# Optimization experiments

Measured on AMD Instinct MI355X. Metric: run time of the kernel, lower is better.

Reference implementation:

```python
import jax, jax.numpy as jnp
import numpy as np

N, E, H, S, F = 50000, 800000, 96, 48, 24


def _mlp(x, W1, b1, W2, b2):
    # equinox MLP depth=1: Linear -> relu -> Linear (identity final activation)
    h = jax.nn.relu(x @ W1.T + b1)
    return h @ W2.T + b2


def _segment_softmax(scores, seg, num_segments):
    mx = jax.ops.segment_max(scores, seg, num_segments=num_segments)
    e = jnp.exp(scores - mx[seg])
    s = jax.ops.segment_sum(e, seg, num_segments=num_segments)
    return e / (s[seg] + 1e-9)


def setup_inputs() -> dict:
    key = jax.random.key(0)
    ks = jax.random.split(key, 32)
    def p(i, shape):
        return jax.random.normal(ks[i], shape, dtype=jnp.float32) * 0.05
    in_attn = 2 * H + 2 * S + F   # 312
    w_attn = 2 * H                # 192
    gin = 3 * H                   # 288
    inp = {
        "x": p(0, (N, H)),
        "x_s": p(1, (N, S)),
        "edge_features": p(2, (E, F)),
        "edge_index": jax.random.randint(ks[3], (2, E), 0, N),
        # fwd attention MLP: in_attn -> w_attn -> 1
        "fwd_W1": p(4, (w_attn, in_attn)), "fwd_b1": p(5, (w_attn,)),
        "fwd_W2": p(6, (1, w_attn)), "fwd_b2": p(7, (1,)),
        # rev gate MLP: in_attn -> w_attn -> 1
        "rev_W1": p(8, (w_attn, in_attn)), "rev_b1": p(9, (w_attn,)),
        "rev_W2": p(10, (1, w_attn)), "rev_b2": p(11, (1,)),
        # reset gate MLP: 3H -> 3H -> H
        "reset_W1": p(12, (gin, gin)), "reset_b1": p(13, (gin,)),
        "reset_W2": p(14, (H, gin)), "reset_b2": p(15, (H,)),
        # update gate MLP: 3H -> 3H -> H
        "update_W1": p(16, (gin, gin)), "update_b1": p(17, (gin,)),
        "update_W2": p(18, (H, gin)), "update_b2": p(19, (H,)),
        # candidate MLP: 3H -> 3H -> H
        "cand_W1": p(20, (gin, gin)), "cand_b1": p(21, (gin,)),
        "cand_W2": p(22, (H, gin)), "cand_b2": p(23, (H,)),
    }
    return inp


def reference(x, x_s, edge_features, edge_index,
              fwd_W1, fwd_b1, fwd_W2, fwd_b2,
              rev_W1, rev_b1, rev_W2, rev_b2,
              reset_W1, reset_b1, reset_W2, reset_b2,
              update_W1, update_b1, update_W2, update_b2,
              cand_W1, cand_b1, cand_W2, cand_b2):
    num_nodes = x.shape[0]
    src, dest = edge_index[0], edge_index[1]

    def compute_messages(s, d, W1, b1, W2, b2, use_softmax):
        feat = jnp.concatenate([x[s], x[d], x_s[s], x_s[d], edge_features], axis=-1)
        raw = _mlp(feat, W1, b1, W2, b2)[:, 0]  # [E]
        if use_softmax:
            raw = jax.nn.leaky_relu(raw) / jnp.sqrt(jnp.asarray(x.shape[-1], dtype=x.dtype))
            w = _segment_softmax(raw, d, num_nodes)
        else:
            w = jax.nn.sigmoid(raw)
        agg = jax.ops.segment_sum(x[s] * w[:, None], d, num_segments=num_nodes)
        return agg, w

    fwd_msgs, fwd_w = compute_messages(src, dest, fwd_W1, fwd_b1, fwd_W2, fwd_b2, True)
    rev_msgs, rev_w = compute_messages(dest, src, rev_W1, rev_b1, rev_W2, rev_b2, False)

    messages = jnp.concatenate([fwd_msgs, rev_msgs], axis=-1)  # [N, 2H]
    gate_input = jnp.concatenate([x, messages], axis=-1)        # [N, 3H]
    r_gate = jax.nn.sigmoid(_mlp(gate_input, reset_W1, reset_b1, reset_W2, reset_b2))
    z_gate = jax.nn.sigmoid(_mlp(gate_input, update_W1, update_b1, update_W2, update_b2))
    cand_input = jnp.concatenate([r_gate * x, messages], axis=-1)
    candidate = jnp.tanh(_mlp(cand_input, cand_W1, cand_b1, cand_W2, cand_b2))
    update = (1 - z_gate) * x + z_gate * candidate
    return (update, fwd_w, rev_w, z_gate, r_gate)
```

## Files before the change

kernel.cpp:

```cpp
#include <hip/hip_runtime.h>
#include <math.h>

typedef unsigned short u16;
typedef unsigned int   u32;

#define HDIM 96
#define SDIM 48
#define FDIM 24
#define KA   312
#define WATT 192
#define KG   288

#define AS_E  328
#define KT_A  10
#define KT_G  9
#define NS    296

#define NFRAG (2 * KT_A * 12 * 64)
#define W1F_Q (KT_G * 18 * 64)
#define W2F_Q (KT_G * 6 * 64)
#define NODEF_Q (3 * (W1F_Q + W2F_Q))

typedef __attribute__((ext_vector_type(8))) __bf16 bf16x8;
typedef __attribute__((ext_vector_type(4))) float  f32x4;

__device__ __forceinline__ u16 f2bf(float f) {
  u32 u = __float_as_uint(f);
  u = (u + 0x7FFFu + ((u >> 16) & 1u)) >> 16;
  return (u16)u;
}
__device__ __forceinline__ float bf2f(u16 v) {
  return __uint_as_float((u32)v << 16);
}
__device__ __forceinline__ u32 pack2(float a, float b) {
  return (u32)f2bf(a) | ((u32)f2bf(b) << 16);
}
__device__ __forceinline__ f32x4 mfma_bf16(bf16x8 a, bf16x8 b, f32x4 c) {
  return __builtin_amdgcn_mfma_f32_16x16x32_bf16(a, b, c, 0, 0, 0);
}

__global__ __launch_bounds__(256) void w_prep(
    const float* __restrict__ fW1, const float* __restrict__ rW1,
    uint4* __restrict__ Bfrag)
{
  const int idx = blockIdx.x * 256 + threadIdx.x;
  if (idx >= NFRAG) return;
  const int lane = idx & 63;
  const int frag = idx >> 6;
  const int nt   = frag % 12;
  const int rest = frag / 12;
  const int kt   = rest % KT_A;
  const int mlp  = rest / KT_A;
  const int q = lane >> 4, c = lane & 15;
  const int n  = nt * 16 + c;
  const int p0 = kt * 16 + q * 4;
  const float* W = mlp ? rW1 : fW1;
  u32 v[4];
#pragma unroll
  for (int w = 0; w < 4; ++w) {
    const int p = p0 + w;
    u32 val = 0u;
    if (p < 156) {
      int src = p;
      if (mlp) {
        if (src < 48)       src += 48;
        else if (src < 96)  src -= 48;
        else if (src < 120) src += 24;
        else if (src < 144) src -= 24;
      }
      const float2 wv = *(const float2*)(W + (size_t)n * KA + 2 * src);
      val = pack2(wv.x, wv.y);
    }
    v[w] = val;
  }
  Bfrag[idx] = make_uint4(v[0], v[1], v[2], v[3]);
}

__global__ __launch_bounds__(256) void w_prep_node(
    const float* __restrict__ W, uint4* __restrict__ outf, int NT)
{
  const int nfrag = KT_G * NT * 64;
  const int idx = blockIdx.x * 256 + threadIdx.x;
  if (idx >= nfrag) return;
  const int lane = idx & 63;
  const int frag = idx >> 6;
  const int nt = frag % NT, kt = frag / NT;
  const int q = lane >> 4, c = lane & 15;
  const int n = nt * 16 + c;
  const int k0 = kt * 32 + q * 8;
  u32 v[4];
#pragma unroll
  for (int w = 0; w < 4; ++w) {
    const float2 wv = *(const float2*)(W + (size_t)n * KG + k0 + 2 * w);
    v[w] = pack2(wv.x, wv.y);
  }
  outf[idx] = make_uint4(v[0], v[1], v[2], v[3]);
}

__global__ __launch_bounds__(256) void x_prep(
    const float* __restrict__ x, const float* __restrict__ xs,
    u32* __restrict__ xb, u32* __restrict__ xsb, int N)
{
  const int i = blockIdx.x * 256 + threadIdx.x;
  const int nx = N * 48;
  if (i < nx) {
    const float2 v = ((const float2*)x)[i];
    xb[i] = pack2(v.x, v.y);
  } else if (i < nx + N * 24) {
    const float2 v = ((const float2*)xs)[i - nx];
    xsb[i - nx] = pack2(v.x, v.y);
  }
}

__global__ __launch_bounds__(256, 2) void edge_kernel(
    const u32* __restrict__ xb, const u32* __restrict__ xsb,
    const float* __restrict__ ef, const int* __restrict__ ei,
    const u16* __restrict__ Bfrag,
    const float* __restrict__ fb1, const float* __restrict__ fW2,
    const float* __restrict__ fb2,
    const float* __restrict__ rb1, const float* __restrict__ rW2,
    const float* __restrict__ rb2,
    float* __restrict__ pe, float* __restrict__ out_revw, int N, int E)
{
  __shared__ __align__(16) u16 Alds[64 * AS_E];
  __shared__ float red[4][64];

  const int tid  = threadIdx.x;
  const int wave = tid >> 6, lane = tid & 63;
  const int q = lane >> 4, c = lane & 15;
  const int e0 = blockIdx.x * 64;

  {
    const int el = tid >> 2, sub = tid & 3;
    const int e = min(e0 + el, E - 1);
    int s = ei[e], d = ei[(size_t)E + e];
    s = min(max(s, 0), N - 1); d = min(max(d, 0), N - 1);
    const uint4* xsr = (const uint4*)(xb  + (size_t)s * 48);
    const uint4* xdr = (const uint4*)(xb  + (size_t)d * 48);
    const uint4* ssr = (const uint4*)(xsb + (size_t)s * 24);
    const uint4* sdr = (const uint4*)(xsb + (size_t)d * 24);
    uint4* Arow = (uint4*)&Alds[el * AS_E];
    uint4 v[10];
    if (sub == 0) {
#pragma unroll
      for (int i = 0; i < 10; ++i) v[i] = xsr[i];
    } else if (sub == 1) {
      v[0] = xsr[10]; v[1] = xsr[11];
#pragma unroll
      for (int i = 0; i < 8; ++i) v[2 + i] = xdr[i];
    } else if (sub == 2) {
#pragma unroll
      for (int i = 0; i < 4; ++i) v[i] = xdr[8 + i];
#pragma unroll
      for (int i = 0; i < 6; ++i) v[4 + i] = ssr[i];
    } else {
#pragma unroll
      for (int i = 0; i < 6; ++i) v[i] = sdr[i];
      const float4* efr = (const float4*)(ef + (size_t)e * 24);
#pragma unroll
      for (int u = 0; u < 3; ++u) {
        const float4 a = efr[2 * u], b = efr[2 * u + 1];
        v[6 + u] = make_uint4(pack2(a.x, a.y), pack2(a.z, a.w),
                              pack2(b.x, b.y), pack2(b.z, b.w));
      }
      v[9] = make_uint4(0u, 0u, 0u, 0u);
    }
#pragma unroll
    for (int i = 0; i < 10; ++i) Arow[sub * 10 + i] = v[i];
  }
  __syncthreads();

  const bf16x8* __restrict__ Bf = (const bf16x8*)Bfrag;

  for (int mlp = 0; mlp < 2; ++mlp) {
    f32x4 acc[4][3];
#pragma unroll
    for (int m = 0; m < 4; ++m)
      for (int t = 0; t < 3; ++t)
        acc[m][t] = (f32x4){0.f, 0.f, 0.f, 0.f};

#pragma unroll
    for (int kt = 0; kt < KT_A; ++kt) {
      bf16x8 a[4];
#pragma unroll
      for (int m = 0; m < 4; ++m)
        a[m] = *(const bf16x8*)&Alds[(m * 16 + c) * AS_E + kt * 32 + q * 8];
#pragma unroll
      for (int t = 0; t < 3; ++t) {
        const bf16x8 b =
            Bf[(((mlp * KT_A + kt) * 12) + wave * 3 + t) * 64 + lane];
#pragma unroll
        for (int m = 0; m < 4; ++m)
          acc[m][t] = mfma_bf16(a[m], b, acc[m][t]);
      }
    }

    const float* b1p = mlp ? rb1 : fb1;
    const float* W2p = mlp ? rW2 : fW2;
    float p[4][4];
#pragma unroll
    for (int m = 0; m < 4; ++m)
      for (int r = 0; r < 4; ++r) p[m][r] = 0.f;
#pragma unroll
    for (int t = 0; t < 3; ++t) {
      const int n = (wave * 3 + t) * 16 + c;
      const float b1f = b1p[n];
      const float w2f = W2p[n];
#pragma unroll
      for (int m = 0; m < 4; ++m)
        for (int r = 0; r < 4; ++r) {
          float h = acc[m][t][r] + b1f;
          h = h > 0.f ? h : 0.f;
          p[m][r] += h * w2f;
        }
    }
    for (int off = 1; off <= 8; off <<= 1)
#pragma unroll
      for (int m = 0; m < 4; ++m)
        for (int r = 0; r < 4; ++r)
          p[m][r] += __shfl_xor(p[m][r], off, 64);

    __syncthreads();
    if (c == 0) {
#pragma unroll
      for (int m = 0; m < 4; ++m)
        for (int r = 0; r < 4; ++r)
          red[wave][m * 16 + q * 4 + r] = p[m][r];
    }
    __syncthreads();

    if (tid < 64 && e0 + tid < E) {
      float raw = red[0][tid] + red[1][tid] + red[2][tid] + red[3][tid];
      const int e = e0 + tid;
      if (mlp == 0) {
        raw += fb2[0];
        const float lr = raw > 0.f ? raw : 0.01f * raw;
        pe[e] = __expf(lr * 0.10206207261596575f);
      } else {
        raw += rb2[0];
        out_revw[e] = 1.f / (1.f + __expf(-raw));
      }
    }
  }
}

__global__ __launch_bounds__(256) void k_hist(
    const int* __restrict__ ei, int* __restrict__ deg_d,
    int* __restrict__ deg_s, int N, int E)
{
  const int e = blockIdx.x * 256 + threadIdx.x;
  if (e >= E) return;
  const int s = min(max(ei[e], 0), N - 1);
  const int d = min(max(ei[(size_t)E + e], 0), N - 1);
  atomicAdd(&deg_d[d], 1);
  atomicAdd(&deg_s[s], 1);
}

__global__ __launch_bounds__(256) void k_scan1(
    const int* __restrict__ deg_d, const int* __restrict__ deg_s,
    int* __restrict__ start_d, int* __restrict__ start_s,
    int* __restrict__ bsum_d, int* __restrict__ bsum_s, int N)
{
  __shared__ int sh[256];
  const int t = threadIdx.x, i = blockIdx.x * 256 + t;
  {
    const int v = (i < N) ? deg_d[i] : 0;
    sh[t] = v; __syncthreads();
    for (int off = 1; off < 256; off <<= 1) {
      const int u = (t >= off) ? sh[t - off] : 0;
      __syncthreads();
      sh[t] += u;
      __syncthreads();
    }
    if (i < N) start_d[i] = sh[t] - v;
    if (t == 255) bsum_d[blockIdx.x] = sh[255];
    __syncthreads();
  }
  {
    const int v = (i < N) ? deg_s[i] : 0;
    sh[t] = v; __syncthreads();
    for (int off = 1; off < 256; off <<= 1) {
      const int u = (t >= off) ? sh[t - off] : 0;
      __syncthreads();
      sh[t] += u;
      __syncthreads();
    }
    if (i < N) start_s[i] = sh[t] - v;
    if (t == 255) bsum_s[blockIdx.x] = sh[255];
  }
}

__global__ void k_scan2(int* bsum_d, int* bsum_s, int nb) {
  if (threadIdx.x == 0) {
    int r = 0;
    for (int b = 0; b < nb; ++b) { const int t = bsum_d[b]; bsum_d[b] = r; r += t; }
  } else if (threadIdx.x == 1) {
    int r = 0;
    for (int b = 0; b < nb; ++b) { const int t = bsum_s[b]; bsum_s[b] = r; r += t; }
  }
}

__global__ __launch_bounds__(256) void k_scan3(
    int* __restrict__ start_d, int* __restrict__ start_s,
    const int* __restrict__ bsum_d, const int* __restrict__ bsum_s,
    int* __restrict__ pos_d, int* __restrict__ pos_s, int N)
{
  const int i = blockIdx.x * 256 + threadIdx.x;
  if (i >= N) return;
  const int b = i >> 8;
  const int vd = start_d[i] + bsum_d[b]; start_d[i] = vd; pos_d[i] = vd;
  const int vs = start_s[i] + bsum_s[b]; start_s[i] = vs; pos_s[i] = vs;
}

__global__ __launch_bounds__(256) void k_fill(
    const int* __restrict__ ei, int* __restrict__ pos_d,
    int* __restrict__ pos_s, int* __restrict__ eidx_d,
    int* __restrict__ eidx_s, int N, int E)
{
  const int e = blockIdx.x * 256 + threadIdx.x;
  if (e >= E) return;
  const int s = min(max(ei[e], 0), N - 1);
  const int d = min(max(ei[(size_t)E + e], 0), N - 1);
  eidx_d[atomicAdd(&pos_d[d], 1)] = e;
  eidx_s[atomicAdd(&pos_s[s], 1)] = e;
}

template <int DIR>
__global__ __launch_bounds__(256) void k_agg(
    const float* __restrict__ x, const int* __restrict__ ei,
    const float* __restrict__ pe, const float* __restrict__ revw,
    const int* __restrict__ start, const int* __restrict__ endp,
    const int* __restrict__ eidx,
    u16* __restrict__ outm, float* __restrict__ out_fwdw, int N, int E)
{
  const int g = threadIdx.x >> 5;
  const int l = threadIdx.x & 31;
  const int n = blockIdx.x * 8 + g;
  if (n >= N) return;
  const int beg = start[n], end = endp[n];

  float inv = 1.f;
  if (DIR == 0) {
    float sum = 0.f;
    for (int i = beg + l; i < end; i += 32) sum += pe[eidx[i]];
    for (int off = 16; off; off >>= 1) sum += __shfl_xor(sum, off, 32);
    inv = 1.f / (sum + 1e-9f);
    for (int i = beg + l; i < end; i += 32) {
      const int e = eidx[i];
      out_fwdw[e] = pe[e] * inv;
    }
  }

  float a0 = 0.f, a1 = 0.f, a2 = 0.f;
  for (int i = beg; i < end; ++i) {
    const int e = eidx[i];
    const float w = (DIR == 0) ? pe[e] * inv : revw[e];
    const int o = (DIR == 0) ? min(max(ei[e], 0), N - 1)
                             : min(max(ei[(size_t)E + e], 0), N - 1);
    const float* xr = x + (size_t)o * 96;
    a0 += w * xr[l];
    a1 += w * xr[l + 32];
    a2 += w * xr[l + 64];
  }
  u16* orow = outm + (size_t)n * 96;
  orow[l] = f2bf(a0); orow[l + 32] = f2bf(a1); orow[l + 64] = f2bf(a2);
}

__device__ __forceinline__ void node_mlp(
    const u16* __restrict__ Alds, u16* __restrict__ Hlds,
    const bf16x8* __restrict__ W1f, const bf16x8* __restrict__ W2f,
    const float* __restrict__ b1,
    int wave, int lane, int q, int c, int ntc, int ntc2,
    f32x4 (&acc2)[4][2])
{
  f32x4 acc[4][5];
#pragma unroll
  for (int m = 0; m < 4; ++m)
    for (int t = 0; t < 5; ++t) acc[m][t] = (f32x4){0.f, 0.f, 0.f, 0.f};

#pragma unroll
  for (int kt = 0; kt < KT_G; ++kt) {
    bf16x8 a[4];
#pragma unroll
    for (int m = 0; m < 4; ++m)
      a[m] = *(const bf16x8*)&Alds[(m * 16 + c) * NS + kt * 32 + q * 8];
#pragma unroll
    for (int t = 0; t < 5; ++t) {
      if (t < ntc) {
        const int nt = wave + 4 * t;
        const bf16x8 b = W1f[(kt * 18 + nt) * 64 + lane];
#pragma unroll
        for (int m = 0; m < 4; ++m)
          acc[m][t] = mfma_bf16(a[m], b, acc[m][t]);
      }
    }
  }

  __syncthreads();
#pragma unroll
  for (int t = 0; t < 5; ++t) {
    if (t < ntc) {
      const int n = (wave + 4 * t) * 16 + c;
      const float b1f = b1[n];
#pragma unroll
      for (int m = 0; m < 4; ++m)
        for (int r = 0; r < 4; ++r) {
          float h = acc[m][t][r] + b1f;
          h = h > 0.f ? h : 0.f;
          Hlds[(m * 16 + q * 4 + r) * NS + n] = f2bf(h);
        }
    }
  }
  __syncthreads();

#pragma unroll
  for (int m = 0; m < 4; ++m)
    for (int t = 0; t < 2; ++t) acc2[m][t] = (f32x4){0.f, 0.f, 0.f, 0.f};
#pragma unroll
  for (int kt = 0; kt < KT_G; ++kt) {
    bf16x8 a[4];
#pragma unroll
    for (int m = 0; m < 4; ++m)
      a[m] = *(const bf16x8*)&Hlds[(m * 16 + c) * NS + kt * 32 + q * 8];
#pragma unroll
    for (int t = 0; t < 2; ++t) {
      if (t < ntc2) {
        const int nt = wave + 4 * t;
        const bf16x8 b = W2f[(kt * 6 + nt) * 64 + lane];
#pragma unroll
        for (int m = 0; m < 4; ++m)
          acc2[m][t] = mfma_bf16(a[m], b, acc2[m][t]);
      }
    }
  }
}

__global__ __launch_bounds__(256, 2) void node_fused(
    const float* __restrict__ x, const u32* __restrict__ xb,
    const u32* __restrict__ fwdmb, const u32* __restrict__ revmb,
    const uint4* __restrict__ NodeF,
    const float* __restrict__ b1r, const float* __restrict__ b2r,
    const float* __restrict__ b1u, const float* __restrict__ b2u,
    const float* __restrict__ b1c, const float* __restrict__ b2c,
    float* __restrict__ out_r, float* __restrict__ out_z,
    float* __restrict__ out_upd, int N)
{
  __shared__ __align__(16) u16 Alds[64 * NS];
  __shared__ __align__(16) u16 Hlds[64 * NS];

  const int tid = threadIdx.x;
  const int wave = tid >> 6, lane = tid & 63;
  const int q = lane >> 4, c = lane & 15;
  const int n0 = blockIdx.x * 64;
  const int ntc  = (wave < 2) ? 5 : 4;
  const int ntc2 = (wave < 2) ? 2 : 1;

  {
    const int nl = tid >> 2, sub = tid & 3;
    const int node = min(n0 + nl, N - 1);
    const uint4* xr = (const uint4*)(xb    + (size_t)node * 48);
    const uint4* fr = (const uint4*)(fwdmb + (size_t)node * 48);
    const uint4* rr = (const uint4*)(revmb + (size_t)node * 48);
    uint4* Arow = (uint4*)&Alds[nl * NS];
    uint4 v[9];
    if (sub == 0) {
#pragma unroll
      for (int i = 0; i < 9; ++i) v[i] = xr[i];
    } else if (sub == 1) {
      v[0] = xr[9]; v[1] = xr[10]; v[2] = xr[11];
#pragma unroll
      for (int i = 0; i < 6; ++i) v[3 + i] = fr[i];
    } else if (sub == 2) {
#pragma unroll
      for (int i = 0; i < 6; ++i) v[i] = fr[6 + i];
      v[6] = rr[0]; v[7] = rr[1]; v[8] = rr[2];
    } else {
#pragma unroll
      for (int i = 0; i < 9; ++i) v[i] = rr[3 + i];
    }
#pragma unroll
    for (int i = 0; i < 9; ++i) Arow[sub * 9 + i] = v[i];
  }
  __syncthreads();

  const bf16x8* W1fr = (const bf16x8*)(NodeF);
  const bf16x8* W2fr = (const bf16x8*)(NodeF + W1F_Q);
  const bf16x8* W1fu = (const bf16x8*)(NodeF + W1F_Q + W2F_Q);
  const bf16x8* W2fu = (const bf16x8*)(NodeF + 2 * W1F_Q + W2F_Q);
  const bf16x8* W1fc = (const bf16x8*)(NodeF + 2 * (W1F_Q + W2F_Q));
  const bf16x8* W2fc = (const bf16x8*)(NodeF + 3 * W1F_Q + 2 * W2F_Q);

  f32x4 acc2[4][2];

  node_mlp(Alds, Hlds, W1fr, W2fr, b1r, wave, lane, q, c, ntc, ntc2, acc2);
  float r_reg[2][4][4];
#pragma unroll
  for (int t = 0; t < 2; ++t) {
    if (t < ntc2) {
      const int n2 = (wave + 4 * t) * 16 + c;
      const float b2f = b2r[n2];
#pragma unroll
      for (int m = 0; m < 4; ++m)
        for (int r = 0; r < 4; ++r) {
          const float v = acc2[m][t][r] + b2f;
          const float rv = 1.f / (1.f + __expf(-v));
          r_reg[t][m][r] = rv;
          const int node = n0 + m * 16 + q * 4 + r;
          if (node < N) out_r[(size_t)node * HDIM + n2] = rv;
        }
    }
  }

  node_mlp(Alds, Hlds, W1fu, W2fu, b1u, wave, lane, q, c, ntc, ntc2, acc2);
  float z_reg[2][4][4];
#pragma unroll
  for (int t = 0; t < 2; ++t) {
    if (t < ntc2) {
      const int n2 = (wave + 4 * t) * 16 + c;
      const float b2f = b2u[n2];
#pragma unroll
      for (int m = 0; m < 4; ++m)
        for (int r = 0; r < 4; ++r) {
          const float v = acc2[m][t][r] + b2f;
          const float zv = 1.f / (1.f + __expf(-v));
          z_reg[t][m][r] = zv;
          const int node = n0 + m * 16 + q * 4 + r;
          if (node < N) out_z[(size_t)node * HDIM + n2] = zv;
        }
    }
  }

#pragma unroll
  for (int t = 0; t < 2; ++t) {
    if (t < ntc2) {
      const int n2 = (wave + 4 * t) * 16 + c;
#pragma unroll
      for (int m = 0; m < 4; ++m)
        for (int r = 0; r < 4; ++r) {
          const int row = m * 16 + q * 4 + r;
          const int idx = row * NS + n2;
          Alds[idx] = f2bf(bf2f(Alds[idx]) * r_reg[t][m][r]);
        }
    }
  }
  __syncthreads();

  node_mlp(Alds, Hlds, W1fc, W2fc, b1c, wave, lane, q, c, ntc, ntc2, acc2);
#pragma unroll
  for (int t = 0; t < 2; ++t) {
    if (t < ntc2) {
      const int n2 = (wave + 4 * t) * 16 + c;
      const float b2f = b2c[n2];
#pragma unroll
      for (int m = 0; m < 4; ++m)
        for (int r = 0; r < 4; ++r) {
          const int node = n0 + m * 16 + q * 4 + r;
          if (node < N) {
            const float v = acc2[m][t][r] + b2f;
            const float ct = tanhf(v);
            const float z = z_reg[t][m][r];
            const float xv = x[(size_t)node * HDIM + n2];
            out_upd[(size_t)node * HDIM + n2] = (1.f - z) * xv + z * ct;
          }
        }
    }
  }
}

__global__ void sentinel_kernel(float* out, int n, float val) {
  const int i = blockIdx.x * 256 + threadIdx.x;
  if (i < n) out[i] = val;
}

extern "C" void kernel_launch(void* const* d_in, const int* in_sizes, int n_in,
                              void* d_out, int out_size, void* d_ws, size_t ws_size,
                              hipStream_t stream) {
  const float* x  = (const float*)d_in[0];
  const float* xs = (const float*)d_in[1];
  const float* ef = (const float*)d_in[2];
  const int*   ei = (const int*)d_in[3];

  const int N = in_sizes[0] / HDIM;
  const int E = in_sizes[3] / 2;

  float* out = (float*)d_out;

  const int NB = (N + 255) / 256;

  const bool sizes_ok =
      n_in == 24 && NB <= 1024 &&
      in_sizes[0] == N * HDIM && in_sizes[1] == N * SDIM &&
      in_sizes[2] == E * FDIM && in_sizes[3] == 2 * E &&
      in_sizes[4] == WATT * KA && in_sizes[5] == WATT &&
      in_sizes[6] == WATT && in_sizes[7] == 1 &&
      in_sizes[12] == KG * KG && in_sizes[13] == KG &&
      in_sizes[14] == HDIM * KG && in_sizes[15] == HDIM &&
      out_size == 3 * N * HDIM + 2 * E;
  if (!sizes_ok) {
    sentinel_kernel<<<(out_size + 255) / 256, 256, 0, stream>>>(out, out_size, 777.0f);
    return;
  }

  const size_t eA = ((size_t)E + 3) & ~(size_t)3;
  const size_t needed =
      (eA + (size_t)NFRAG * 4 + (size_t)NODEF_Q * 4 +
       (size_t)N * 48 + (size_t)N * 24 + 2 * (size_t)N * 48 +
       6 * (size_t)N + 2048 + 2 * (size_t)E) * 4;
  if (ws_size < needed) {
    sentinel_kernel<<<(out_size + 255) / 256, 256, 0, stream>>>(out, out_size, 12345.0f);
    return;
  }
  float* pe    = (float*)d_ws;
  uint4* Bfrag = (uint4*)((u32*)d_ws + eA);
  uint4* NodeF = Bfrag + NFRAG;
  u32*   xbw   = (u32*)(NodeF + NODEF_Q);
  u32*   xsbw  = xbw + (size_t)N * 48;
  u32*   fwdmb = xsbw + (size_t)N * 24;
  u32*   revmb = fwdmb + (size_t)N * 48;
  int* deg_d   = (int*)(revmb + (size_t)N * 48);
  int* deg_s   = deg_d + N;
  int* start_d = deg_s + N;
  int* start_s = start_d + N;
  int* pos_d   = start_s + N;
  int* pos_s   = pos_d + N;
  int* bsum_d  = pos_s + N;
  int* bsum_s  = bsum_d + 1024;
  int* eidx_d  = bsum_s + 1024;
  int* eidx_s  = eidx_d + E;

  float* out_update = out;
  float* out_fwdw   = out + (size_t)N * HDIM;
  float* out_revw   = out_fwdw + E;
  float* out_z      = out_revw + E;
  float* out_r      = out_z + (size_t)N * HDIM;

  (void)hipMemsetAsync(deg_d, 0, 2 * (size_t)N * sizeof(int), stream);

  w_prep<<<(NFRAG + 255) / 256, 256, 0, stream>>>(
      (const float*)d_in[4], (const float*)d_in[8], Bfrag);
  const int g1 = (KT_G * 18 * 64 + 255) / 256;
  const int g2 = (KT_G * 6 * 64 + 255) / 256;
  w_prep_node<<<g1, 256, 0, stream>>>((const float*)d_in[12], NodeF, 18);
  w_prep_node<<<g2, 256, 0, stream>>>((const float*)d_in[14], NodeF + W1F_Q, 6);
  w_prep_node<<<g1, 256, 0, stream>>>((const float*)d_in[16],
                                      NodeF + W1F_Q + W2F_Q, 18);
  w_prep_node<<<g2, 256, 0, stream>>>((const float*)d_in[18],
                                      NodeF + 2 * W1F_Q + W2F_Q, 6);
  w_prep_node<<<g1, 256, 0, stream>>>((const float*)d_in[20],
                                      NodeF + 2 * (W1F_Q + W2F_Q), 18);
  w_prep_node<<<g2, 256, 0, stream>>>((const float*)d_in[22],
                                      NodeF + 3 * W1F_Q + 2 * W2F_Q, 6);
  x_prep<<<(N * 72 + 255) / 256, 256, 0, stream>>>(x, xs, xbw, xsbw, N);

  const int eblk = (E + 255) / 256;
  k_hist<<<eblk, 256, 0, stream>>>(ei, deg_d, deg_s, N, E);
  k_scan1<<<NB, 256, 0, stream>>>(deg_d, deg_s, start_d, start_s,
                                  bsum_d, bsum_s, N);
  k_scan2<<<1, 64, 0, stream>>>(bsum_d, bsum_s, NB);
  k_scan3<<<NB, 256, 0, stream>>>(start_d, start_s, bsum_d, bsum_s,
                                  pos_d, pos_s, N);
  k_fill<<<eblk, 256, 0, stream>>>(ei, pos_d, pos_s, eidx_d, eidx_s, N, E);

  edge_kernel<<<(E + 63) / 64, 256, 0, stream>>>(
      xbw, xsbw, ef, ei, (const u16*)Bfrag,
      (const float*)d_in[5], (const float*)d_in[6], (const float*)d_in[7],
      (const float*)d_in[9], (const float*)d_in[10], (const float*)d_in[11],
      pe, out_revw, N, E);

  const int ablk = (N + 7) / 8;
  k_agg<0><<<ablk, 256, 0, stream>>>(x, ei, pe, out_revw, start_d, pos_d,
                                     eidx_d, (u16*)fwdmb, out_fwdw, N, E);
  k_agg<1><<<ablk, 256, 0, stream>>>(x, ei, pe, out_revw, start_s, pos_s,
                                     eidx_s, (u16*)revmb, out_fwdw, N, E);

  const int nblk = (N + 63) / 64;
  node_fused<<<nblk, 256, 0, stream>>>(
      x, xbw, fwdmb, revmb, NodeF,
      (const float*)d_in[13], (const float*)d_in[15],
      (const float*)d_in[17], (const float*)d_in[19],
      (const float*)d_in[21], (const float*)d_in[23],
      out_r, out_z, out_update, N);
}
```

Before: 1.131 ms.

## Merge prep and aggregation launches, fuse edge MLPs, load edge A-operands directly

Combines the eight weight/activation prep kernels into one launch and the two aggregation directions into one grid. The scan2 kernel is removed by having each scan3 block sum the preceding block totals itself. The edge kernel now computes the forward and reverse MLPs in one K-loop that shares A fragments, and it loads those fragments straight from global memory instead of staging them in LDS. This saves launches, barriers and LDS traffic, but doubles the accumulator registers and replaces coalesced staging with scattered 16-byte gathers per lane.

```diff
diff --git a/kernel.cpp b/kernel.cpp
--- a/kernel.cpp
+++ b/kernel.cpp
@@ -11,7 +11,6 @@
 #define WATT 192
 #define KG   288
 
-#define AS_E  328
 #define KT_A  10
 #define KT_G  9
 #define NS    296
@@ -21,6 +20,11 @@
 #define W2F_Q (KT_G * 6 * 64)
 #define NODEF_Q (3 * (W1F_Q + W2F_Q))
 
+#define PB_EDGE 60
+#define PB_W1   41
+#define PB_W2   14
+#define PB_NODE (3 * (PB_W1 + PB_W2))
+
 typedef __attribute__((ext_vector_type(8))) __bf16 bf16x8;
 typedef __attribute__((ext_vector_type(4))) float  f32x4;
 
@@ -39,76 +43,97 @@
   return __builtin_amdgcn_mfma_f32_16x16x32_bf16(a, b, c, 0, 0, 0);
 }
 
-__global__ __launch_bounds__(256) void w_prep(
+__global__ __launch_bounds__(256) void prep_all(
     const float* __restrict__ fW1, const float* __restrict__ rW1,
-    uint4* __restrict__ Bfrag)
-{
-  const int idx = blockIdx.x * 256 + threadIdx.x;
-  if (idx >= NFRAG) return;
-  const int lane = idx & 63;
-  const int frag = idx >> 6;
-  const int nt   = frag % 12;
-  const int rest = frag / 12;
-  const int kt   = rest % KT_A;
-  const int mlp  = rest / KT_A;
-  const int q = lane >> 4, c = lane & 15;
-  const int n  = nt * 16 + c;
-  const int p0 = kt * 16 + q * 4;
-  const float* W = mlp ? rW1 : fW1;
-  u32 v[4];
-#pragma unroll
-  for (int w = 0; w < 4; ++w) {
-    const int p = p0 + w;
-    u32 val = 0u;
-    if (p < 156) {
-      int src = p;
-      if (mlp) {
-        if (src < 48)       src += 48;
-        else if (src < 96)  src -= 48;
-        else if (src < 120) src += 24;
-        else if (src < 144) src -= 24;
-      }
-      const float2 wv = *(const float2*)(W + (size_t)n * KA + 2 * src);
-      val = pack2(wv.x, wv.y);
-    }
-    v[w] = val;
-  }
-  Bfrag[idx] = make_uint4(v[0], v[1], v[2], v[3]);
-}
-
-__global__ __launch_bounds__(256) void w_prep_node(
-    const float* __restrict__ W, uint4* __restrict__ outf, int NT)
-{
-  const int nfrag = KT_G * NT * 64;
-  const int idx = blockIdx.x * 256 + threadIdx.x;
-  if (idx >= nfrag) return;
-  const int lane = idx & 63;
-  const int frag = idx >> 6;
-  const int nt = frag % NT, kt = frag / NT;
-  const int q = lane >> 4, c = lane & 15;
-  const int n = nt * 16 + c;
-  const int k0 = kt * 32 + q * 8;
-  u32 v[4];
-#pragma unroll
-  for (int w = 0; w < 4; ++w) {
-    const float2 wv = *(const float2*)(W + (size_t)n * KG + k0 + 2 * w);
-    v[w] = pack2(wv.x, wv.y);
-  }
-  outf[idx] = make_uint4(v[0], v[1], v[2], v[3]);
-}
-
-__global__ __launch_bounds__(256) void x_prep(
+    uint4* __restrict__ Bfrag,
+    const float* __restrict__ W1r, const float* __restrict__ W2r,
+    const float* __restrict__ W1u, const float* __restrict__ W2u,
+    const float* __restrict__ W1c, const float* __restrict__ W2c,
+    uint4* __restrict__ NodeF,
     const float* __restrict__ x, const float* __restrict__ xs,
     u32* __restrict__ xb, u32* __restrict__ xsb, int N)
 {
-  const int i = blockIdx.x * 256 + threadIdx.x;
-  const int nx = N * 48;
-  if (i < nx) {
-    const float2 v = ((const float2*)x)[i];
-    xb[i] = pack2(v.x, v.y);
-  } else if (i < nx + N * 24) {
-    const float2 v = ((const float2*)xs)[i - nx];
-    xsb[i - nx] = pack2(v.x, v.y);
+  int b = blockIdx.x;
+  const int tid = threadIdx.x;
+
+  if (b < PB_EDGE) {
+    const int idx = b * 256 + tid;
+    const int lane = idx & 63;
+    const int frag = idx >> 6;
+    const int nt   = frag % 12;
+    const int rest = frag / 12;
+    const int kt   = rest % KT_A;
+    const int mlp  = rest / KT_A;
+    const int q = lane >> 4, c = lane & 15;
+    const int n  = nt * 16 + c;
+    const int p0 = kt * 16 + q * 4;
+    const float* W = mlp ? rW1 : fW1;
+    u32 v[4];
+#pragma unroll
+    for (int w = 0; w < 4; ++w) {
+      const int p = p0 + w;
+      u32 val = 0u;
+      if (p < 156) {
+        int src = p;
+        if (mlp) {
+          if (src < 48)       src += 48;
+          else if (src < 96)  src -= 48;
+          else if (src < 120) src += 24;
+          else if (src < 144) src -= 24;
+        }
+        const float2 wv = *(const float2*)(W + (size_t)n * KA + 2 * src);
+        val = pack2(wv.x, wv.y);
+      }
+      v[w] = val;
+    }
+    Bfrag[idx] = make_uint4(v[0], v[1], v[2], v[3]);
+    return;
+  }
+  b -= PB_EDGE;
+
+  if (b < PB_NODE) {
+    const int mlp = b / (PB_W1 + PB_W2);
+    const int lb  = b % (PB_W1 + PB_W2);
+    const float* W;
+    uint4* o;
+    int NT, idx;
+    if (lb < PB_W1) {
+      NT = 18; idx = lb * 256 + tid;
+      W = (mlp == 0) ? W1r : (mlp == 1) ? W1u : W1c;
+      o = NodeF + (size_t)mlp * (W1F_Q + W2F_Q);
+    } else {
+      NT = 6; idx = (lb - PB_W1) * 256 + tid;
+      W = (mlp == 0) ? W2r : (mlp == 1) ? W2u : W2c;
+      o = NodeF + (size_t)mlp * (W1F_Q + W2F_Q) + W1F_Q;
+    }
+    if (idx >= KT_G * NT * 64) return;
+    const int lane = idx & 63;
+    const int frag = idx >> 6;
+    const int nt = frag % NT, kt = frag / NT;
+    const int q = lane >> 4, c = lane & 15;
+    const int n = nt * 16 + c;
+    const int k0 = kt * 32 + q * 8;
+    u32 v[4];
+#pragma unroll
+    for (int w = 0; w < 4; ++w) {
+      const float2 wv = *(const float2*)(W + (size_t)n * KG + k0 + 2 * w);
+      v[w] = pack2(wv.x, wv.y);
+    }
+    o[idx] = make_uint4(v[0], v[1], v[2], v[3]);
+    return;
+  }
+  b -= PB_NODE;
+
+  {
+    const int i = b * 256 + tid;
+    const int nx = N * 48;
+    if (i < nx) {
+      const float2 v = ((const float2*)x)[i];
+      xb[i] = pack2(v.x, v.y);
+    } else if (i < nx + N * 24) {
+      const float2 v = ((const float2*)xs)[i - nx];
+      xsb[i - nx] = pack2(v.x, v.y);
+    }
   }
 }
 
@@ -122,125 +147,123 @@
     const float* __restrict__ rb2,
     float* __restrict__ pe, float* __restrict__ out_revw, int N, int E)
 {
-  __shared__ __align__(16) u16 Alds[64 * AS_E];
-  __shared__ float red[4][64];
+  __shared__ float red[2][4][64];
 
   const int tid  = threadIdx.x;
   const int wave = tid >> 6, lane = tid & 63;
   const int q = lane >> 4, c = lane & 15;
   const int e0 = blockIdx.x * 64;
 
-  {
-    const int el = tid >> 2, sub = tid & 3;
-    const int e = min(e0 + el, E - 1);
-    int s = ei[e], d = ei[(size_t)E + e];
-    s = min(max(s, 0), N - 1); d = min(max(d, 0), N - 1);
-    const uint4* xsr = (const uint4*)(xb  + (size_t)s * 48);
-    const uint4* xdr = (const uint4*)(xb  + (size_t)d * 48);
-    const uint4* ssr = (const uint4*)(xsb + (size_t)s * 24);
-    const uint4* sdr = (const uint4*)(xsb + (size_t)d * 24);
-    uint4* Arow = (uint4*)&Alds[el * AS_E];
-    uint4 v[10];
-    if (sub == 0) {
-#pragma unroll
-      for (int i = 0; i < 10; ++i) v[i] = xsr[i];
-    } else if (sub == 1) {
-      v[0] = xsr[10]; v[1] = xsr[11];
-#pragma unroll
-      for (int i = 0; i < 8; ++i) v[2 + i] = xdr[i];
-    } else if (sub == 2) {
-#pragma unroll
-      for (int i = 0; i < 4; ++i) v[i] = xdr[8 + i];
-#pragma unroll
-      for (int i = 0; i < 6; ++i) v[4 + i] = ssr[i];
-    } else {
-#pragma unroll
-      for (int i = 0; i < 6; ++i) v[i] = sdr[i];
-      const float4* efr = (const float4*)(ef + (size_t)e * 24);
-#pragma unroll
-      for (int u = 0; u < 3; ++u) {
-        const float4 a = efr[2 * u], b = efr[2 * u + 1];
-        v[6 + u] = make_uint4(pack2(a.x, a.y), pack2(a.z, a.w),
-                              pack2(b.x, b.y), pack2(b.z, b.w));
+  int em[4], sm[4], dm[4];
+#pragma unroll
+  for (int m = 0; m < 4; ++m) {
+    em[m] = min(e0 + m * 16 + c, E - 1);
+    int s = ei[em[m]], d = ei[(size_t)E + em[m]];
+    sm[m] = min(max(s, 0), N - 1);
+    dm[m] = min(max(d, 0), N - 1);
+  }
+
+  const bf16x8* __restrict__ Bf = (const bf16x8*)Bfrag;
+
+  f32x4 accF[4][3], accR[4][3];
+#pragma unroll
+  for (int m = 0; m < 4; ++m)
+    for (int t = 0; t < 3; ++t) {
+      accF[m][t] = (f32x4){0.f, 0.f, 0.f, 0.f};
+      accR[m][t] = (f32x4){0.f, 0.f, 0.f, 0.f};
+    }
+
+#pragma unroll
+  for (int kt = 0; kt < KT_A; ++kt) {
+    const int p0 = kt * 16 + q * 4;
+    bf16x8 a[4];
+#pragma unroll
+    for (int m = 0; m < 4; ++m) {
+      uint4 av;
+      if (kt < 3) {
+        av = *(const uint4*)(xb + (size_t)sm[m] * 48 + p0);
+      } else if (kt < 6) {
+        av = *(const uint4*)(xb + (size_t)dm[m] * 48 + (p0 - 48));
+      } else if (kt == 6) {
+        av = *(const uint4*)(xsb + (size_t)sm[m] * 24 + (p0 - 96));
+      } else if (kt == 7) {
+        const u32* p = (q < 2) ? xsb + (size_t)sm[m] * 24 + (p0 - 96)
+                               : xsb + (size_t)dm[m] * 24 + (p0 - 120);
+        av = *(const uint4*)p;
+      } else if (kt == 8) {
+        av = *(const uint4*)(xsb + (size_t)dm[m] * 24 + (p0 - 120));
+      } else {
+        if (q < 3) {
+          const float* efp = ef + (size_t)em[m] * 24 + (p0 - 144) * 2;
+          const float4 f0 = *(const float4*)efp;
+          const float4 f1 = *(const float4*)(efp + 4);
+          av = make_uint4(pack2(f0.x, f0.y), pack2(f0.z, f0.w),
+                          pack2(f1.x, f1.y), pack2(f1.z, f1.w));
+        } else {
+          av = make_uint4(0u, 0u, 0u, 0u);
+        }
       }
-      v[9] = make_uint4(0u, 0u, 0u, 0u);
-    }
-#pragma unroll
-    for (int i = 0; i < 10; ++i) Arow[sub * 10 + i] = v[i];
+      a[m] = __builtin_bit_cast(bf16x8, av);
+    }
+#pragma unroll
+    for (int t = 0; t < 3; ++t) {
+      const bf16x8 bF = Bf[((kt * 12) + wave * 3 + t) * 64 + lane];
+      const bf16x8 bR = Bf[(((KT_A + kt) * 12) + wave * 3 + t) * 64 + lane];
+#pragma unroll
+      for (int m = 0; m < 4; ++m) {
+        accF[m][t] = mfma_bf16(a[m], bF, accF[m][t]);
+        accR[m][t] = mfma_bf16(a[m], bR, accR[m][t]);
+      }
+    }
+  }
+
+  float pf[4][4], pr[4][4];
+#pragma unroll
+  for (int m = 0; m < 4; ++m)
+    for (int r = 0; r < 4; ++r) { pf[m][r] = 0.f; pr[m][r] = 0.f; }
+#pragma unroll
+  for (int t = 0; t < 3; ++t) {
+    const int n = (wave * 3 + t) * 16 + c;
+    const float fb = fb1[n], fw = fW2[n];
+    const float rb = rb1[n], rw = rW2[n];
+#pragma unroll
+    for (int m = 0; m < 4; ++m)
+      for (int r = 0; r < 4; ++r) {
+        float hf = accF[m][t][r] + fb;
+        hf = hf > 0.f ? hf : 0.f;
+        pf[m][r] += hf * fw;
+        float hr = accR[m][t][r] + rb;
+        hr = hr > 0.f ? hr : 0.f;
+        pr[m][r] += hr * rw;
+      }
+  }
+  for (int off = 1; off <= 8; off <<= 1)
+#pragma unroll
+    for (int m = 0; m < 4; ++m)
+      for (int r = 0; r < 4; ++r) {
+        pf[m][r] += __shfl_xor(pf[m][r], off, 64);
+        pr[m][r] += __shfl_xor(pr[m][r], off, 64);
+      }
+
+  if (c == 0) {
+#pragma unroll
+    for (int m = 0; m < 4; ++m)
+      for (int r = 0; r < 4; ++r) {
+        red[0][wave][m * 16 + q * 4 + r] = pf[m][r];
+        red[1][wave][m * 16 + q * 4 + r] = pr[m][r];
+      }
   }
   __syncthreads();
 
-  const bf16x8* __restrict__ Bf = (const bf16x8*)Bfrag;
-
-  for (int mlp = 0; mlp < 2; ++mlp) {
-    f32x4 acc[4][3];
-#pragma unroll
-    for (int m = 0; m < 4; ++m)
-      for (int t = 0; t < 3; ++t)
-        acc[m][t] = (f32x4){0.f, 0.f, 0.f, 0.f};
-
-#pragma unroll
-    for (int kt = 0; kt < KT_A; ++kt) {
-      bf16x8 a[4];
-#pragma unroll
-      for (int m = 0; m < 4; ++m)
-        a[m] = *(const bf16x8*)&Alds[(m * 16 + c) * AS_E + kt * 32 + q * 8];
-#pragma unroll
-      for (int t = 0; t < 3; ++t) {
-        const bf16x8 b =
-            Bf[(((mlp * KT_A + kt) * 12) + wave * 3 + t) * 64 + lane];
-#pragma unroll
-        for (int m = 0; m < 4; ++m)
-          acc[m][t] = mfma_bf16(a[m], b, acc[m][t]);
-      }
-    }
-
-    const float* b1p = mlp ? rb1 : fb1;
-    const float* W2p = mlp ? rW2 : fW2;
-    float p[4][4];
-#pragma unroll
-    for (int m = 0; m < 4; ++m)
-      for (int r = 0; r < 4; ++r) p[m][r] = 0.f;
-#pragma unroll
-    for (int t = 0; t < 3; ++t) {
-      const int n = (wave * 3 + t) * 16 + c;
-      const float b1f = b1p[n];
-      const float w2f = W2p[n];
-#pragma unroll
-      for (int m = 0; m < 4; ++m)
-        for (int r = 0; r < 4; ++r) {
-          float h = acc[m][t][r] + b1f;
-          h = h > 0.f ? h : 0.f;
-          p[m][r] += h * w2f;
-        }
-    }
-    for (int off = 1; off <= 8; off <<= 1)
-#pragma unroll
-      for (int m = 0; m < 4; ++m)
-        for (int r = 0; r < 4; ++r)
-          p[m][r] += __shfl_xor(p[m][r], off, 64);
-
-    __syncthreads();
-    if (c == 0) {
-#pragma unroll
-      for (int m = 0; m < 4; ++m)
-        for (int r = 0; r < 4; ++r)
-          red[wave][m * 16 + q * 4 + r] = p[m][r];
-    }
-    __syncthreads();
-
-    if (tid < 64 && e0 + tid < E) {
-      float raw = red[0][tid] + red[1][tid] + red[2][tid] + red[3][tid];
-      const int e = e0 + tid;
-      if (mlp == 0) {
-        raw += fb2[0];
-        const float lr = raw > 0.f ? raw : 0.01f * raw;
-        pe[e] = __expf(lr * 0.10206207261596575f);
-      } else {
-        raw += rb2[0];
-        out_revw[e] = 1.f / (1.f + __expf(-raw));
-      }
-    }
+  if (tid < 64 && e0 + tid < E) {
+    const int e = e0 + tid;
+    float rawf = red[0][0][tid] + red[0][1][tid] + red[0][2][tid] + red[0][3][tid];
+    rawf += fb2[0];
+    const float lr = rawf > 0.f ? rawf : 0.01f * rawf;
+    pe[e] = __expf(lr * 0.10206207261596575f);
+    float rawr = red[1][0][tid] + red[1][1][tid] + red[1][2][tid] + red[1][3][tid];
+    rawr += rb2[0];
+    out_revw[e] = 1.f / (1.f + __expf(-rawr));
   }
 }
 
@@ -290,26 +313,24 @@
   }
 }
 
-__global__ void k_scan2(int* bsum_d, int* bsum_s, int nb) {
-  if (threadIdx.x == 0) {
-    int r = 0;
-    for (int b = 0; b < nb; ++b) { const int t = bsum_d[b]; bsum_d[b] = r; r += t; }
-  } else if (threadIdx.x == 1) {
-    int r = 0;
-    for (int b = 0; b < nb; ++b) { const int t = bsum_s[b]; bsum_s[b] = r; r += t; }
-  }
-}
-
 __global__ __launch_bounds__(256) void k_scan3(
     int* __restrict__ start_d, int* __restrict__ start_s,
     const int* __restrict__ bsum_d, const int* __restrict__ bsum_s,
     int* __restrict__ pos_d, int* __restrict__ pos_s, int N)
 {
-  const int i = blockIdx.x * 256 + threadIdx.x;
+  __shared__ int offs[2];
+  const int t = threadIdx.x;
+  if (t < 2) {
+    const int* bs = t ? bsum_s : bsum_d;
+    int r = 0;
+    for (int bb = 0; bb < (int)blockIdx.x; ++bb) r += bs[bb];
+    offs[t] = r;
+  }
+  __syncthreads();
+  const int i = blockIdx.x * 256 + t;
   if (i >= N) return;
-  const int b = i >> 8;
-  const int vd = start_d[i] + bsum_d[b]; start_d[i] = vd; pos_d[i] = vd;
-  const int vs = start_s[i] + bsum_s[b]; start_s[i] = vs; pos_s[i] = vs;
+  const int vd = start_d[i] + offs[0]; start_d[i] = vd; pos_d[i] = vd;
+  const int vs = start_s[i] + offs[1]; start_s[i] = vs; pos_s[i] = vs;
 }
 
 __global__ __launch_bounds__(256) void k_fill(
@@ -325,22 +346,31 @@
   eidx_s[atomicAdd(&pos_s[s], 1)] = e;
 }
 
-template <int DIR>
-__global__ __launch_bounds__(256) void k_agg(
+__global__ __launch_bounds__(256) void k_agg_all(
     const float* __restrict__ x, const int* __restrict__ ei,
     const float* __restrict__ pe, const float* __restrict__ revw,
-    const int* __restrict__ start, const int* __restrict__ endp,
-    const int* __restrict__ eidx,
-    u16* __restrict__ outm, float* __restrict__ out_fwdw, int N, int E)
-{
+    const int* __restrict__ start_d, const int* __restrict__ end_d,
+    const int* __restrict__ eidx_d,
+    const int* __restrict__ start_s, const int* __restrict__ end_s,
+    const int* __restrict__ eidx_s,
+    u16* __restrict__ fwdm, u16* __restrict__ revm,
+    float* __restrict__ out_fwdw, int N, int E, int ablk)
+{
+  int b = blockIdx.x;
+  const int dir = (b >= ablk) ? 1 : 0;
+  if (dir) b -= ablk;
   const int g = threadIdx.x >> 5;
   const int l = threadIdx.x & 31;
-  const int n = blockIdx.x * 8 + g;
+  const int n = b * 8 + g;
   if (n >= N) return;
+
+  const int* start = dir ? start_s : start_d;
+  const int* endp  = dir ? end_s   : end_d;
+  const int* eidx  = dir ? eidx_s  : eidx_d;
   const int beg = start[n], end = endp[n];
 
   float inv = 1.f;
-  if (DIR == 0) {
+  if (dir == 0) {
     float sum = 0.f;
     for (int i = beg + l; i < end; i += 32) sum += pe[eidx[i]];
     for (int off = 16; off; off >>= 1) sum += __shfl_xor(sum, off, 32);
@@ -354,15 +384,15 @@
   float a0 = 0.f, a1 = 0.f, a2 = 0.f;
   for (int i = beg; i < end; ++i) {
     const int e = eidx[i];
-    const float w = (DIR == 0) ? pe[e] * inv : revw[e];
-    const int o = (DIR == 0) ? min(max(ei[e], 0), N - 1)
+    const float w = (dir == 0) ? pe[e] * inv : revw[e];
+    const int o = (dir == 0) ? min(max(ei[e], 0), N - 1)
                              : min(max(ei[(size_t)E + e], 0), N - 1);
     const float* xr = x + (size_t)o * 96;
     a0 += w * xr[l];
     a1 += w * xr[l + 32];
     a2 += w * xr[l + 64];
   }
-  u16* orow = outm + (size_t)n * 96;
+  u16* orow = (dir ? revm : fwdm) + (size_t)n * 96;
   orow[l] = f2bf(a0); orow[l + 32] = f2bf(a1); orow[l + 64] = f2bf(a2);
 }
 
@@ -462,24 +492,30 @@
     const uint4* fr = (const uint4*)(fwdmb + (size_t)node * 48);
     const uint4* rr = (const uint4*)(revmb + (size_t)node * 48);
     uint4* Arow = (uint4*)&Alds[nl * NS];
-    uint4 v[9];
     if (sub == 0) {
-#pragma unroll
-      for (int i = 0; i < 9; ++i) v[i] = xr[i];
+      uint4 t0 = xr[0], t1 = xr[1], t2 = xr[2], t3 = xr[3], t4 = xr[4],
+            t5 = xr[5], t6 = xr[6], t7 = xr[7], t8 = xr[8];
+      Arow[0] = t0; Arow[1] = t1; Arow[2] = t2; Arow[3] = t3; Arow[4] = t4;
+      Arow[5] = t5; Arow[6] = t6; Arow[7] = t7; Arow[8] = t8;
     } else if (sub == 1) {
-      v[0] = xr[9]; v[1] = xr[10]; v[2] = xr[11];
-#pragma unroll
-      for (int i = 0; i < 6; ++i) v[3 + i] = fr[i];
+      uint4 t0 = xr[9], t1 = xr[10], t2 = xr[11], t3 = fr[0], t4 = fr[1],
+            t5 = fr[2], t6 = fr[3], t7 = fr[4], t8 = fr[5];
+      Arow[9] = t0; Arow[10] = t1; Arow[11] = t2; Arow[12] = t3;
+      Arow[13] = t4; Arow[14] = t5; Arow[15] = t6; Arow[16] = t7;
+      Arow[17] = t8;
     } else if (sub == 2) {
-#pragma unroll
-      for (int i = 0; i < 6; ++i) v[i] = fr[6 + i];
-      v[6] = rr[0]; v[7] = rr[1]; v[8] = rr[2];
+      uint4 t0 = fr[6], t1 = fr[7], t2 = fr[8], t3 = fr[9], t4 = fr[10],
+            t5 = fr[11], t6 = rr[0], t7 = rr[1], t8 = rr[2];
+      Arow[18] = t0; Arow[19] = t1; Arow[20] = t2; Arow[21] = t3;
+      Arow[22] = t4; Arow[23] = t5; Arow[24] = t6; Arow[25] = t7;
+      Arow[26] = t8;
     } else {
-#pragma unroll
-      for (int i = 0; i < 9; ++i) v[i] = rr[3 + i];
-    }
-#pragma unroll
-    for (int i = 0; i < 9; ++i) Arow[sub * 9 + i] = v[i];
+      uint4 t0 = rr[3], t1 = rr[4], t2 = rr[5], t3 = rr[6], t4 = rr[7],
+            t5 = rr[8], t6 = rr[9], t7 = rr[10], t8 = rr[11];
+      Arow[27] = t0; Arow[28] = t1; Arow[29] = t2; Arow[30] = t3;
+      Arow[31] = t4; Arow[32] = t5; Arow[33] = t6; Arow[34] = t7;
+      Arow[35] = t8;
+    }
   }
   __syncthreads();
 
@@ -636,27 +672,18 @@
 
   (void)hipMemsetAsync(deg_d, 0, 2 * (size_t)N * sizeof(int), stream);
 
-  w_prep<<<(NFRAG + 255) / 256, 256, 0, stream>>>(
-      (const float*)d_in[4], (const float*)d_in[8], Bfrag);
-  const int g1 = (KT_G * 18 * 64 + 255) / 256;
-  const int g2 = (KT_G * 6 * 64 + 255) / 256;
-  w_prep_node<<<g1, 256, 0, stream>>>((const float*)d_in[12], NodeF, 18);
-  w_prep_node<<<g2, 256, 0, stream>>>((const float*)d_in[14], NodeF + W1F_Q, 6);
-  w_prep_node<<<g1, 256, 0, stream>>>((const float*)d_in[16],
-                                      NodeF + W1F_Q + W2F_Q, 18);
-  w_prep_node<<<g2, 256, 0, stream>>>((const float*)d_in[18],
-                                      NodeF + 2 * W1F_Q + W2F_Q, 6);
-  w_prep_node<<<g1, 256, 0, stream>>>((const float*)d_in[20],
-                                      NodeF + 2 * (W1F_Q + W2F_Q), 18);
-  w_prep_node<<<g2, 256, 0, stream>>>((const float*)d_in[22],
-                                      NodeF + 3 * W1F_Q + 2 * W2F_Q, 6);
-  x_prep<<<(N * 72 + 255) / 256, 256, 0, stream>>>(x, xs, xbw, xsbw, N);
+  const int prep_blocks = PB_EDGE + PB_NODE + (N * 72 + 255) / 256;
+  prep_all<<<prep_blocks, 256, 0, stream>>>(
+      (const float*)d_in[4], (const float*)d_in[8], Bfrag,
+      (const float*)d_in[12], (const float*)d_in[14],
+      (const float*)d_in[16], (const float*)d_in[18],
+      (const float*)d_in[20], (const float*)d_in[22], NodeF,
+      x, xs, xbw, xsbw, N);
 
   const int eblk = (E + 255) / 256;
   k_hist<<<eblk, 256, 0, stream>>>(ei, deg_d, deg_s, N, E);
   k_scan1<<<NB, 256, 0, stream>>>(deg_d, deg_s, start_d, start_s,
                                   bsum_d, bsum_s, N);
-  k_scan2<<<1, 64, 0, stream>>>(bsum_d, bsum_s, NB);
   k_scan3<<<NB, 256, 0, stream>>>(start_d, start_s, bsum_d, bsum_s,
                                   pos_d, pos_s, N);
   k_fill<<<eblk, 256, 0, stream>>>(ei, pos_d, pos_s, eidx_d, eidx_s, N, E);
@@ -668,10 +695,10 @@
       pe, out_revw, N, E);
 
   const int ablk = (N + 7) / 8;
-  k_agg<0><<<ablk, 256, 0, stream>>>(x, ei, pe, out_revw, start_d, pos_d,
-                                     eidx_d, (u16*)fwdmb, out_fwdw, N, E);
-  k_agg<1><<<ablk, 256, 0, stream>>>(x, ei, pe, out_revw, start_s, pos_s,
-                                     eidx_s, (u16*)revmb, out_fwdw, N, E);
+  k_agg_all<<<2 * ablk, 256, 0, stream>>>(
+      x, ei, pe, out_revw,
+      start_d, pos_d, eidx_d, start_s, pos_s, eidx_s,
+      (u16*)fwdmb, (u16*)revmb, out_fwdw, N, E, ablk);
 
   const int nblk = (N + 63) / 64;
   node_fused<<<nblk, 256, 0, stream>>>(
```

Result: no change. 1.111 ms (-1.8%).
